# Kernel optimization log

Measured on AMD Instinct MI355X. Metric: run time of the kernel, lower is better.

## Reference

```python
import jax, jax.numpy as jnp
import numpy as np

B, N, S, C1, C2 = 8, 8192, 2048, 128, 256
H1, H2 = 256, 256
EPS_LN = 1e-5


def _layernorm_c(x, g, b):
    # LayerNorm over channel dim of [B, C, N]
    mu = jnp.mean(x, axis=1, keepdims=True)
    var = jnp.mean((x - mu) ** 2, axis=1, keepdims=True)
    return g[None, :, None] * (x - mu) / jnp.sqrt(var + EPS_LN) + b[None, :, None]


def setup_inputs() -> dict:
    key = jax.random.key(0)
    ks = jax.random.split(key, 8)
    Cin = C1 + C2
    return {
        "points_coor1": jax.random.normal(ks[0], (B, 3, N), jnp.float32),
        "points_coor2": jax.random.normal(ks[1], (B, 3, S), jnp.float32),
        "points_fea1": jax.random.normal(ks[2], (B, C1, N), jnp.float32),
        "points_fea2": jax.random.normal(ks[3], (B, C2, S), jnp.float32),
        "points_padding2": jnp.zeros((B, S), dtype=bool),
        "W1": jax.random.normal(ks[4], (H1, Cin), jnp.float32) * 0.05,
        "b1": jnp.zeros((H1,), jnp.float32),
        "g1": jnp.ones((H1,), jnp.float32),
        "be1": jnp.zeros((H1,), jnp.float32),
        "W2": jax.random.normal(ks[5], (H2, H1), jnp.float32) * 0.05,
        "b2": jnp.zeros((H2,), jnp.float32),
        "g2": jnp.ones((H2,), jnp.float32),
        "be2": jnp.zeros((H2,), jnp.float32),
    }


def reference(points_coor1, points_coor2, points_fea1, points_fea2,
              points_padding2, W1, b1, g1, be1, W2, b2, g2, be2):
    c1 = jnp.transpose(points_coor1, (0, 2, 1))  # [B,N,3]
    c2 = jnp.transpose(points_coor2, (0, 2, 1))  # [B,S,3]
    f2 = jnp.transpose(points_fea2, (0, 2, 1))   # [B,S,C2]

    # push padded points far away (max computed on unmodified coords, as in torch RHS-first eval)
    big = jnp.max(jnp.abs(c2)) * 3.0
    c2 = jnp.where(points_padding2[..., None], big, c2)

    # squared euclidean pairwise distances [B,N,S]
    d = (jnp.sum(c1 * c1, -1)[:, :, None]
         + jnp.sum(c2 * c2, -1)[:, None, :]
         - 2.0 * jnp.einsum('bnd,bsd->bns', c1, c2))

    neg_d, idx = jax.lax.top_k(-d, 3)          # 3 smallest distances
    dists = -neg_d                              # [B,N,3]
    recip = 1.0 / jnp.clip(dists, 1e-8)
    w = recip / jnp.sum(recip, axis=-1, keepdims=True)  # [B,N,3]

    gathered = jax.vmap(lambda f, i: f[i])(f2, idx)     # [B,N,3,C2]
    interp = jnp.einsum('bnkc,bnk->bcn', gathered, w)   # [B,C2,N]

    x = jnp.concatenate([points_fea1, interp], axis=1)  # [B,C1+C2,N]
    x = jax.nn.relu(_layernorm_c(jnp.einsum('oc,bcn->bon', W1, x) + b1[None, :, None], g1, be1))
    x = jax.nn.relu(_layernorm_c(jnp.einsum('oc,bcn->bon', W2, x) + b2[None, :, None], g2, be2))
    return x
```

## Files before the change

### kernel.cpp

```cpp
#include <hip/hip_runtime.h>
#include <stdint.h>

#define BB 8
#define NPT 8192
#define SPT 2048
#define C1D 128
#define C2D 256
#define CIN 384
#define HD 256
#define SPLIT 8
#define SC (SPT/SPLIT)

typedef __attribute__((ext_vector_type(8))) short bf16x8;
typedef __attribute__((ext_vector_type(4))) float f32x4;

__device__ __forceinline__ unsigned short f2b(float f){
  unsigned int u = __float_as_uint(f);
  u += 0x7fffu + ((u >> 16) & 1u);
  return (unsigned short)(u >> 16);
}

__device__ __forceinline__ void bar_sync(){
  __builtin_amdgcn_sched_barrier(0);
  asm volatile("s_waitcnt lgkmcnt(0)" ::: "memory");
  __builtin_amdgcn_s_barrier();
  __builtin_amdgcn_sched_barrier(0);
}

__global__ __launch_bounds__(256) void gsrc_kernel(const float* __restrict__ coor2,
    const unsigned char* __restrict__ pad, float4* __restrict__ gs){
  int i = blockIdx.x * 256 + threadIdx.x;
  int b = i >> 11, s = i & (SPT - 1);
  const float* cb = coor2 + b * 3 * SPT;
  float x = cb[s], y = cb[SPT + s], z = cb[2*SPT + s];
  if (pad[i]) { x = 1e19f; y = 1e19f; z = 1e19f; }
  float n2 = __fadd_rn(__fadd_rn(__fmul_rn(x,x), __fmul_rn(y,y)), __fmul_rn(z,z));
  gs[i] = make_float4(x, y, z, n2);
}

#define NB_KNN 2048
#define NB_CVT 640
#define NB_T2 4096
#define NB_T1 8192
__global__ __launch_bounds__(256) void main_kernel(
    const float* __restrict__ coor1, const float4* __restrict__ gs,
    float* __restrict__ cv, int* __restrict__ cj,
    const float* __restrict__ W1, const float* __restrict__ W2, unsigned short* __restrict__ Wb,
    const float* __restrict__ fea2, unsigned short* __restrict__ f2t,
    const float* __restrict__ fea1, unsigned short* __restrict__ xpm){
  __shared__ unsigned short t[32][33];
  int bid = blockIdx.x, tid = threadIdx.x;
  if (bid < NB_KNN){
    int x = bid & 31, b = (bid >> 5) & 7, c = bid >> 8;
    int s0c = c * SC;
    const float4* gsb = gs + b * SPT + s0c;
    int n = x * 256 + tid;
    const float* ca = coor1 + b * 3 * NPT;
    float x1 = ca[n], y1 = ca[NPT + n], z1 = ca[2*NPT + n];
    float n1 = __fadd_rn(__fadd_rn(__fmul_rn(x1,x1), __fmul_rn(y1,y1)), __fmul_rn(z1,z1));
    float v0 = 3.4e38f, v1 = 3.4e38f, v2 = 3.4e38f;
    int j0 = 0, j1 = 0, j2 = 0;
    #pragma unroll 8
    for (int s = 0; s < SC; s++){
      float4 q = gsb[s];
      float dot = __fadd_rn(__fadd_rn(__fmul_rn(x1,q.x), __fmul_rn(y1,q.y)), __fmul_rn(z1,q.z));
      float npn = __fadd_rn(n1, q.w);
      float d = __builtin_fmaf(-2.0f, dot, npn);
      bool l0 = d < v0, l1 = d < v1, l2 = d < v2;
      j2 = l1 ? j1 : (l2 ? s : j2);
      j1 = l0 ? j0 : (l1 ? s : j1);
      j0 = l0 ? s  : j0;
      float nv2 = __builtin_amdgcn_fmed3f(v1, v2, d);
      float nv1 = __builtin_amdgcn_fmed3f(v0, v1, d);
      v0 = fminf(v0, d); v1 = nv1; v2 = nv2;
    }
    size_t m = (size_t)b * NPT + n;
    size_t base = (m * SPLIT + c) * 3;
    cv[base+0] = v0; cv[base+1] = v1; cv[base+2] = v2;
    cj[base+0] = s0c + j0; cj[base+1] = s0c + j1; cj[base+2] = s0c + j2;
    return;
  }
  bid -= NB_KNN;
  if (bid < NB_CVT){
    int i = bid * 256 + tid;
    const int n1 = HD * CIN;
    if (i < n1) Wb[i] = f2b(W1[i]);
    else { int k = i - n1; if (k < HD * HD) Wb[n1 + k] = f2b(W2[k]); }
    return;
  }
  bid -= NB_CVT;
  const float* src; unsigned short* dst; int Cdim, Ndim, dstStride, n0, c0, b;
  if (bid < NB_T2){
    src = fea2; dst = f2t; Cdim = C2D; Ndim = SPT; dstStride = C2D;
    n0 = (bid & 63) * 32; c0 = ((bid >> 6) & 7) * 32; b = bid >> 9;
  } else {
    bid -= NB_T2;
    src = fea1; dst = xpm; Cdim = C1D; Ndim = NPT; dstStride = CIN;
    n0 = (bid & 255) * 32; c0 = ((bid >> 8) & 3) * 32; b = bid >> 10;
  }
  int tx = tid & 31, ty = tid >> 5;
  const float* s = src + (size_t)b * Cdim * Ndim;
  unsigned short* d = dst + (size_t)b * Ndim * dstStride;
  #pragma unroll
  for (int i = 0; i < 4; i++)
    t[ty + i*8][tx] = f2b(s[(size_t)(c0 + ty + i*8) * Ndim + n0 + tx]);
  __syncthreads();
  #pragma unroll
  for (int i = 0; i < 4; i++)
    d[(size_t)(n0 + ty + i*8) * dstStride + c0 + tx] = t[tx][ty + i*8];
}

__global__ __launch_bounds__(256) void knn_merge_kernel(const float* __restrict__ cv,
    const int* __restrict__ cj, float* __restrict__ w3, int* __restrict__ i3){
  size_t m = (size_t)blockIdx.x * 256 + threadIdx.x;
  float v0 = 3.4e38f, v1 = 3.4e38f, v2 = 3.4e38f;
  int j0 = 0, j1 = 0, j2 = 0;
  #pragma unroll
  for (int c = 0; c < SPLIT; c++){
    #pragma unroll
    for (int k = 0; k < 3; k++){
      float d = cv[(m * SPLIT + c) * 3 + k];
      int j   = cj[(m * SPLIT + c) * 3 + k];
      bool l0 = d < v0, l1 = d < v1, l2 = d < v2;
      j2 = l1 ? j1 : (l2 ? j : j2);
      j1 = l0 ? j0 : (l1 ? j : j1);
      j0 = l0 ? j  : j0;
      float nv2 = __builtin_amdgcn_fmed3f(v1, v2, d);
      float nv1 = __builtin_amdgcn_fmed3f(v0, v1, d);
      v0 = fminf(v0, d); v1 = nv1; v2 = nv2;
    }
  }
  float r0 = 1.0f / fmaxf(v0, 1e-8f);
  float r1 = 1.0f / fmaxf(v1, 1e-8f);
  float r2 = 1.0f / fmaxf(v2, 1e-8f);
  float rs = (r0 + r1) + r2;
  w3[m*3+0] = r0 / rs; w3[m*3+1] = r1 / rs; w3[m*3+2] = r2 / rs;
  i3[m*3+0] = j0; i3[m*3+1] = j1; i3[m*3+2] = j2;
}

__global__ __launch_bounds__(256) void interp_kernel(const unsigned short* __restrict__ f2t,
    const float* __restrict__ w3, const int* __restrict__ i3, unsigned short* __restrict__ xpm){
  int m = blockIdx.x * 4 + (threadIdx.x >> 6);
  int lane = threadIdx.x & 63;
  int b = m >> 13;
  int s0 = i3[m*3+0], s1 = i3[m*3+1], s2 = i3[m*3+2];
  float w0 = w3[m*3+0], w1 = w3[m*3+1], w2 = w3[m*3+2];
  const ushort4 a = *(const ushort4*)(f2t + (size_t)(b*SPT + s0) * C2D + lane*4);
  const ushort4 c = *(const ushort4*)(f2t + (size_t)(b*SPT + s1) * C2D + lane*4);
  const ushort4 e = *(const ushort4*)(f2t + (size_t)(b*SPT + s2) * C2D + lane*4);
  #define B2F(u) __uint_as_float(((unsigned int)(u)) << 16)
  ushort4 o;
  o.x = f2b(w0*B2F(a.x) + w1*B2F(c.x) + w2*B2F(e.x));
  o.y = f2b(w0*B2F(a.y) + w1*B2F(c.y) + w2*B2F(e.y));
  o.z = f2b(w0*B2F(a.z) + w1*B2F(c.z) + w2*B2F(e.z));
  o.w = f2b(w0*B2F(a.w) + w1*B2F(c.w) + w2*B2F(e.w));
  *(ushort4*)(xpm + (size_t)m * CIN + C1D + lane*4) = o;
}

__global__ __launch_bounds__(256) void mlp_fused_kernel(const unsigned short* __restrict__ xpm,
    const unsigned short* __restrict__ W1g, const unsigned short* __restrict__ W2g,
    const float* __restrict__ b1, const float* __restrict__ g1, const float* __restrict__ be1,
    const float* __restrict__ b2, const float* __restrict__ g2, const float* __restrict__ be2,
    float* __restrict__ outg){
  __shared__ __align__(16) unsigned short Ws[256*40];
  __shared__ __align__(16) unsigned short Hbuf[64*264];
  __shared__ float sB[256], sG[256], sBe[256];
  unsigned short* Xs = Hbuf;
  int tid = threadIdx.x;
  int m0 = blockIdx.x * 64;
  int b = m0 >> 13, n0 = m0 & (NPT - 1);
  sB[tid] = b1[tid]; sG[tid] = g1[tid]; sBe[tid] = be1[tid];
  int w = tid >> 6, lane = tid & 63, col = lane & 15, quad = lane >> 4;
  int ml = w*16 + col;
  int mr = tid >> 2, part = tid & 3;
  const int4* wsrc  = (const int4*)(W1g + (size_t)tid * CIN);
  const int4* xsrc  = (const int4*)(xpm + (size_t)(m0 + mr) * CIN + part*8);
  f32x4 acc[16];
  #pragma unroll
  for (int i = 0; i < 16; i++) acc[i] = (f32x4)0.0f;

  int4 wA0 = wsrc[0], wA1 = wsrc[1], wA2 = wsrc[2], wA3 = wsrc[3];
  int4 xA  = xsrc[0];
  for (int c = 0; c < 12; c++){
    bar_sync();
    {
      int4* d4 = (int4*)(Ws + tid * 40);
      d4[0] = wA0; d4[1] = wA1; d4[2] = wA2; d4[3] = wA3;
      *(int4*)(Xs + mr*40 + part*8) = xA;
    }
    if (c + 1 < 12){
      wA0 = wsrc[(c+1)*4 + 0]; wA1 = wsrc[(c+1)*4 + 1];
      wA2 = wsrc[(c+1)*4 + 2]; wA3 = wsrc[(c+1)*4 + 3];
      xA  = xsrc[(c+1)*4];
    }
    bar_sync();
    bf16x8 bfrag = *(const bf16x8*)(Xs + ml*40 + quad*8);
    #pragma unroll
    for (int ot = 0; ot < 16; ot++){
      bf16x8 afrag = *(const bf16x8*)(Ws + (ot*16 + col)*40 + quad*8);
      acc[ot] = __builtin_amdgcn_mfma_f32_16x16x32_bf16(afrag, bfrag, acc[ot], 0, 0, 0);
    }
  }
  const int4* w2src = (const int4*)(W2g + (size_t)tid * HD);
  int4 v0r = w2src[0], v1r = w2src[1], v2r = w2src[2], v3r = w2src[3];
  float rb2 = b2[tid], rg2 = g2[tid], rbe2 = be2[tid];
  {
    float s1 = 0.f, s2 = 0.f;
    #pragma unroll
    for (int ot = 0; ot < 16; ot++)
      #pragma unroll
      for (int r = 0; r < 4; r++){
        int o = ot*16 + quad*4 + r;
        float v = acc[ot][r] + sB[o];
        acc[ot][r] = v;
        s1 += v; s2 += v*v;
      }
    s1 += __shfl_xor(s1, 16); s1 += __shfl_xor(s1, 32);
    s2 += __shfl_xor(s2, 16); s2 += __shfl_xor(s2, 32);
    float mu = s1 * (1.f/256.f);
    float rinv = rsqrtf(s2 * (1.f/256.f) - mu*mu + 1e-5f);
    bar_sync();
    #pragma unroll
    for (int ot = 0; ot < 16; ot++){
      int ob = ot*16 + quad*4;
      ushort4 hv;
      hv.x = f2b(fmaxf((acc[ot][0] - mu) * rinv * sG[ob+0] + sBe[ob+0], 0.f));
      hv.y = f2b(fmaxf((acc[ot][1] - mu) * rinv * sG[ob+1] + sBe[ob+1], 0.f));
      hv.z = f2b(fmaxf((acc[ot][2] - mu) * rinv * sG[ob+2] + sBe[ob+2], 0.f));
      hv.w = f2b(fmaxf((acc[ot][3] - mu) * rinv * sG[ob+3] + sBe[ob+3], 0.f));
      *(ushort4*)(Hbuf + ml*264 + ot*16 + quad*4) = hv;
    }
  }
  bar_sync();
  sB[tid] = rb2; sG[tid] = rg2; sBe[tid] = rbe2;

  #pragma unroll
  for (int i = 0; i < 16; i++) acc[i] = (f32x4)0.0f;
  for (int c = 0; c < 8; c++){
    bar_sync();
    {
      int4* d4 = (int4*)(Ws + tid * 40);
      d4[0] = v0r; d4[1] = v1r; d4[2] = v2r; d4[3] = v3r;
    }
    if (c + 1 < 8){
      v0r = w2src[(c+1)*4 + 0]; v1r = w2src[(c+1)*4 + 1];
      v2r = w2src[(c+1)*4 + 2]; v3r = w2src[(c+1)*4 + 3];
    }
    bar_sync();
    bf16x8 bfrag = *(const bf16x8*)(Hbuf + ml*264 + c*32 + quad*8);
    #pragma unroll
    for (int ot = 0; ot < 16; ot++){
      bf16x8 afrag = *(const bf16x8*)(Ws + (ot*16 + col)*40 + quad*8);
      acc[ot] = __builtin_amdgcn_mfma_f32_16x16x32_bf16(afrag, bfrag, acc[ot], 0, 0, 0);
    }
  }
  float s1 = 0.f, s2 = 0.f;
  #pragma unroll
  for (int ot = 0; ot < 16; ot++)
    #pragma unroll
    for (int r = 0; r < 4; r++){
      int o = ot*16 + quad*4 + r;
      float v = acc[ot][r] + sB[o];
      acc[ot][r] = v;
      s1 += v; s2 += v*v;
    }
  s1 += __shfl_xor(s1, 16); s1 += __shfl_xor(s1, 32);
  s2 += __shfl_xor(s2, 16); s2 += __shfl_xor(s2, 32);
  float mu = s1 * (1.f/256.f);
  float rinv = rsqrtf(s2 * (1.f/256.f) - mu*mu + 1e-5f);
  size_t obase = (size_t)b * HD * NPT + n0 + w*16 + col;
  #pragma unroll
  for (int ot = 0; ot < 16; ot++)
    #pragma unroll
    for (int r = 0; r < 4; r++){
      int o = ot*16 + quad*4 + r;
      float v = (acc[ot][r] - mu) * rinv * sG[o] + sBe[o];
      outg[obase + (size_t)o * NPT] = fmaxf(v, 0.f);
    }
}

extern "C" void kernel_launch(void* const* d_in, const int* in_sizes, int n_in,
                              void* d_out, int out_size, void* d_ws, size_t ws_size,
                              hipStream_t stream){
  const float* coor1 = (const float*)d_in[0];
  const float* coor2 = (const float*)d_in[1];
  const float* fea1  = (const float*)d_in[2];
  const float* fea2  = (const float*)d_in[3];
  const unsigned char* pad = (const unsigned char*)d_in[4];
  const float* W1  = (const float*)d_in[5];
  const float* b1  = (const float*)d_in[6];
  const float* g1  = (const float*)d_in[7];
  const float* be1 = (const float*)d_in[8];
  const float* W2  = (const float*)d_in[9];
  const float* b2  = (const float*)d_in[10];
  const float* g2  = (const float*)d_in[11];
  const float* be2 = (const float*)d_in[12];
  float* out = (float*)d_out;

  char* ws = (char*)d_ws;
  float* w3            = (float*)(ws + 256);
  int*   i3            = (int*)  (ws + 786688);
  unsigned short* W1b  = (unsigned short*)(ws + 1573120);
  unsigned short* W2b  = (unsigned short*)(ws + 1769728);
  unsigned short* f2t  = (unsigned short*)(ws + 1900800);
  unsigned short* xpm  = (unsigned short*)(ws + 10289408);
  float* cv            = (float*)(ws + 60621056);
  int*   cj            = (int*)  (ws + 60621056 + 6291456);
  float4* gs           = (float4*)(ws + 60621056 + 16777216);

  gsrc_kernel<<<BB*SPT/256, 256, 0, stream>>>(coor2, pad, gs);
  main_kernel<<<NB_KNN + NB_CVT + NB_T2 + NB_T1, 256, 0, stream>>>(
      coor1, gs, cv, cj, W1, W2, W1b, fea2, f2t, fea1, xpm);
  knn_merge_kernel<<<BB*NPT/256, 256, 0, stream>>>(cv, cj, w3, i3);
  interp_kernel<<<BB*NPT/4, 256, 0, stream>>>(f2t, w3, i3, xpm);
  mlp_fused_kernel<<<BB*NPT/64, 256, 0, stream>>>(xpm, W1b, W2b, b1, g1, be1, b2, g2, be2, out);
}
```

Measured before the change: 242.5 us.

## Fuse KNN merge and interpolation into the fused MLP kernel

```diff
diff --git a/kernel.cpp b/kernel.cpp
--- a/kernel.cpp
+++ b/kernel.cpp
@@ -13,6 +13,8 @@
 
 typedef __attribute__((ext_vector_type(8))) short bf16x8;
 typedef __attribute__((ext_vector_type(4))) float f32x4;
+
+#define B2F(u) __uint_as_float(((unsigned int)(u)) << 16)
 
 __device__ __forceinline__ unsigned short f2b(float f){
   unsigned int u = __float_as_uint(f);
@@ -110,91 +112,97 @@
     d[(size_t)(n0 + ty + i*8) * dstStride + c0 + tx] = t[tx][ty + i*8];
 }
 
-__global__ __launch_bounds__(256) void knn_merge_kernel(const float* __restrict__ cv,
-    const int* __restrict__ cj, float* __restrict__ w3, int* __restrict__ i3){
-  size_t m = (size_t)blockIdx.x * 256 + threadIdx.x;
-  float v0 = 3.4e38f, v1 = 3.4e38f, v2 = 3.4e38f;
-  int j0 = 0, j1 = 0, j2 = 0;
-  #pragma unroll
-  for (int c = 0; c < SPLIT; c++){
-    #pragma unroll
-    for (int k = 0; k < 3; k++){
-      float d = cv[(m * SPLIT + c) * 3 + k];
-      int j   = cj[(m * SPLIT + c) * 3 + k];
-      bool l0 = d < v0, l1 = d < v1, l2 = d < v2;
-      j2 = l1 ? j1 : (l2 ? j : j2);
-      j1 = l0 ? j0 : (l1 ? j : j1);
-      j0 = l0 ? j  : j0;
-      float nv2 = __builtin_amdgcn_fmed3f(v1, v2, d);
-      float nv1 = __builtin_amdgcn_fmed3f(v0, v1, d);
-      v0 = fminf(v0, d); v1 = nv1; v2 = nv2;
-    }
-  }
-  float r0 = 1.0f / fmaxf(v0, 1e-8f);
-  float r1 = 1.0f / fmaxf(v1, 1e-8f);
-  float r2 = 1.0f / fmaxf(v2, 1e-8f);
-  float rs = (r0 + r1) + r2;
-  w3[m*3+0] = r0 / rs; w3[m*3+1] = r1 / rs; w3[m*3+2] = r2 / rs;
-  i3[m*3+0] = j0; i3[m*3+1] = j1; i3[m*3+2] = j2;
-}
-
-__global__ __launch_bounds__(256) void interp_kernel(const unsigned short* __restrict__ f2t,
-    const float* __restrict__ w3, const int* __restrict__ i3, unsigned short* __restrict__ xpm){
-  int m = blockIdx.x * 4 + (threadIdx.x >> 6);
-  int lane = threadIdx.x & 63;
-  int b = m >> 13;
-  int s0 = i3[m*3+0], s1 = i3[m*3+1], s2 = i3[m*3+2];
-  float w0 = w3[m*3+0], w1 = w3[m*3+1], w2 = w3[m*3+2];
-  const ushort4 a = *(const ushort4*)(f2t + (size_t)(b*SPT + s0) * C2D + lane*4);
-  const ushort4 c = *(const ushort4*)(f2t + (size_t)(b*SPT + s1) * C2D + lane*4);
-  const ushort4 e = *(const ushort4*)(f2t + (size_t)(b*SPT + s2) * C2D + lane*4);
-  #define B2F(u) __uint_as_float(((unsigned int)(u)) << 16)
-  ushort4 o;
-  o.x = f2b(w0*B2F(a.x) + w1*B2F(c.x) + w2*B2F(e.x));
-  o.y = f2b(w0*B2F(a.y) + w1*B2F(c.y) + w2*B2F(e.y));
-  o.z = f2b(w0*B2F(a.z) + w1*B2F(c.z) + w2*B2F(e.z));
-  o.w = f2b(w0*B2F(a.w) + w1*B2F(c.w) + w2*B2F(e.w));
-  *(ushort4*)(xpm + (size_t)m * CIN + C1D + lane*4) = o;
-}
-
-__global__ __launch_bounds__(256) void mlp_fused_kernel(const unsigned short* __restrict__ xpm,
+__global__ __launch_bounds__(256) void mlp_fused_kernel(
+    const float* __restrict__ cv, const int* __restrict__ cj,
+    const unsigned short* __restrict__ f2t, const unsigned short* __restrict__ xpm,
     const unsigned short* __restrict__ W1g, const unsigned short* __restrict__ W2g,
     const float* __restrict__ b1, const float* __restrict__ g1, const float* __restrict__ be1,
     const float* __restrict__ b2, const float* __restrict__ g2, const float* __restrict__ be2,
     float* __restrict__ outg){
   __shared__ __align__(16) unsigned short Ws[256*40];
   __shared__ __align__(16) unsigned short Hbuf[64*264];
+  __shared__ __align__(16) unsigned short Xs[64*40];
   __shared__ float sB[256], sG[256], sBe[256];
-  unsigned short* Xs = Hbuf;
+  __shared__ float sW3[64*3];
+  __shared__ int   sI3[64*3];
   int tid = threadIdx.x;
   int m0 = blockIdx.x * 64;
   int b = m0 >> 13, n0 = m0 & (NPT - 1);
-  sB[tid] = b1[tid]; sG[tid] = g1[tid]; sBe[tid] = be1[tid];
   int w = tid >> 6, lane = tid & 63, col = lane & 15, quad = lane >> 4;
   int ml = w*16 + col;
   int mr = tid >> 2, part = tid & 3;
   const int4* wsrc  = (const int4*)(W1g + (size_t)tid * CIN);
   const int4* xsrc  = (const int4*)(xpm + (size_t)(m0 + mr) * CIN + part*8);
-  f32x4 acc[16];
-  #pragma unroll
-  for (int i = 0; i < 16; i++) acc[i] = (f32x4)0.0f;
-
   int4 wA0 = wsrc[0], wA1 = wsrc[1], wA2 = wsrc[2], wA3 = wsrc[3];
   int4 xA  = xsrc[0];
+  sB[tid] = b1[tid]; sG[tid] = g1[tid]; sBe[tid] = be1[tid];
+
+  if (tid < 64){
+    size_t m = (size_t)m0 + tid;
+    float v0 = 3.4e38f, v1 = 3.4e38f, v2 = 3.4e38f;
+    int j0 = 0, j1 = 0, j2 = 0;
+    #pragma unroll
+    for (int c = 0; c < SPLIT; c++){
+      #pragma unroll
+      for (int k = 0; k < 3; k++){
+        float d = cv[(m * SPLIT + c) * 3 + k];
+        int j   = cj[(m * SPLIT + c) * 3 + k];
+        bool l0 = d < v0, l1 = d < v1, l2 = d < v2;
+        j2 = l1 ? j1 : (l2 ? j : j2);
+        j1 = l0 ? j0 : (l1 ? j : j1);
+        j0 = l0 ? j  : j0;
+        float nv2 = __builtin_amdgcn_fmed3f(v1, v2, d);
+        float nv1 = __builtin_amdgcn_fmed3f(v0, v1, d);
+        v0 = fminf(v0, d); v1 = nv1; v2 = nv2;
+      }
+    }
+    float r0 = 1.0f / fmaxf(v0, 1e-8f);
+    float r1 = 1.0f / fmaxf(v1, 1e-8f);
+    float r2 = 1.0f / fmaxf(v2, 1e-8f);
+    float rs = (r0 + r1) + r2;
+    sW3[tid*3+0] = r0 / rs; sW3[tid*3+1] = r1 / rs; sW3[tid*3+2] = r2 / rs;
+    sI3[tid*3+0] = j0; sI3[tid*3+1] = j1; sI3[tid*3+2] = j2;
+  }
+  bar_sync();
+
+  {
+    int pbase = w*16;
+    #pragma unroll 4
+    for (int i = 0; i < 16; i++){
+      int p = pbase + i;
+      float w0 = sW3[p*3+0], w1 = sW3[p*3+1], w2 = sW3[p*3+2];
+      int j0 = sI3[p*3+0], j1 = sI3[p*3+1], j2 = sI3[p*3+2];
+      const ushort4 a  = *(const ushort4*)(f2t + (size_t)(b*SPT + j0) * C2D + lane*4);
+      const ushort4 c4 = *(const ushort4*)(f2t + (size_t)(b*SPT + j1) * C2D + lane*4);
+      const ushort4 e  = *(const ushort4*)(f2t + (size_t)(b*SPT + j2) * C2D + lane*4);
+      ushort4 o;
+      o.x = f2b(w0*B2F(a.x) + w1*B2F(c4.x) + w2*B2F(e.x));
+      o.y = f2b(w0*B2F(a.y) + w1*B2F(c4.y) + w2*B2F(e.y));
+      o.z = f2b(w0*B2F(a.z) + w1*B2F(c4.z) + w2*B2F(e.z));
+      o.w = f2b(w0*B2F(a.w) + w1*B2F(c4.w) + w2*B2F(e.w));
+      *(ushort4*)(Hbuf + p*264 + lane*4) = o;
+    }
+  }
+  f32x4 acc[16];
+  #pragma unroll
+  for (int i = 0; i < 16; i++) acc[i] = (f32x4)0.0f;
+
   for (int c = 0; c < 12; c++){
     bar_sync();
     {
       int4* d4 = (int4*)(Ws + tid * 40);
       d4[0] = wA0; d4[1] = wA1; d4[2] = wA2; d4[3] = wA3;
-      *(int4*)(Xs + mr*40 + part*8) = xA;
+      if (c < 4) *(int4*)(Xs + mr*40 + part*8) = xA;
     }
     if (c + 1 < 12){
       wA0 = wsrc[(c+1)*4 + 0]; wA1 = wsrc[(c+1)*4 + 1];
       wA2 = wsrc[(c+1)*4 + 2]; wA3 = wsrc[(c+1)*4 + 3];
-      xA  = xsrc[(c+1)*4];
-    }
-    bar_sync();
-    bf16x8 bfrag = *(const bf16x8*)(Xs + ml*40 + quad*8);
+      if (c + 1 < 4) xA = xsrc[(c+1)*4];
+    }
+    bar_sync();
+    bf16x8 bfrag = (c < 4)
+      ? *(const bf16x8*)(Xs + ml*40 + quad*8)
+      : *(const bf16x8*)(Hbuf + ml*264 + (c-4)*32 + quad*8);
     #pragma unroll
     for (int ot = 0; ot < 16; ot++){
       bf16x8 afrag = *(const bf16x8*)(Ws + (ot*16 + col)*40 + quad*8);
@@ -298,8 +306,6 @@
   float* out = (float*)d_out;
 
   char* ws = (char*)d_ws;
-  float* w3            = (float*)(ws + 256);
-  int*   i3            = (int*)  (ws + 786688);
   unsigned short* W1b  = (unsigned short*)(ws + 1573120);
   unsigned short* W2b  = (unsigned short*)(ws + 1769728);
   unsigned short* f2t  = (unsigned short*)(ws + 1900800);
@@ -311,7 +317,6 @@
   gsrc_kernel<<<BB*SPT/256, 256, 0, stream>>>(coor2, pad, gs);
   main_kernel<<<NB_KNN + NB_CVT + NB_T2 + NB_T1, 256, 0, stream>>>(
       coor1, gs, cv, cj, W1, W2, W1b, fea2, f2t, fea1, xpm);
-  knn_merge_kernel<<<BB*NPT/256, 256, 0, stream>>>(cv, cj, w3, i3);
-  interp_kernel<<<BB*NPT/4, 256, 0, stream>>>(f2t, w3, i3, xpm);
-  mlp_fused_kernel<<<BB*NPT/64, 256, 0, stream>>>(xpm, W1b, W2b, b1, g1, be1, b2, g2, be2, out);
-}
+  mlp_fused_kernel<<<BB*NPT/64, 256, 0, stream>>>(
+      cv, cj, f2t, xpm, W1b, W2b, b1, g1, be1, b2, g2, be2, out);
+}
```

Result: faster. 233.1 us (-3.8%).
